# Kernel optimization log

Hardware: AMD Instinct MI355X
Metric: run time of the kernel (lower is better)

Reference implementation:

```python
import jax, jax.numpy as jnp
import numpy as np

B, T, C, H = 8, 2048, 384, 64

def setup_inputs() -> dict:
    key = jax.random.key(0)
    k1, k2, k3, k4 = jax.random.split(key, 4)
    x = jax.random.normal(k1, (B, T, C), dtype=jnp.float32)
    Wq = jax.random.normal(k2, (C, H), dtype=jnp.float32) * (C ** -0.5)
    Wk = jax.random.normal(k3, (C, H), dtype=jnp.float32) * (C ** -0.5)
    Wv = jax.random.normal(k4, (C, H), dtype=jnp.float32) * (C ** -0.5)
    return {"x": x, "Wq": Wq, "Wk": Wk, "Wv": Wv}

def reference(x, Wq, Wk, Wv):
    # x: (B, T, C); projections: (B, T, H)
    Bn, Tn, Cn = x.shape
    q = jnp.einsum('btc,ch->bth', x, Wq)
    k = jnp.einsum('btc,ch->bth', x, Wk)
    v = jnp.einsum('btc,ch->bth', x, Wv)
    # NOTE: source scales by C**-0.5 (embedding dim), not head_size**-0.5
    weights = jnp.einsum('bth,bsh->bts', q, k) * (Cn ** -0.5)  # (B, T, T)
    causal = jnp.tril(jnp.ones((Tn, Tn), dtype=bool))
    weights = jnp.where(causal, weights, -jnp.inf)
    # NOTE: source applies softmax over dim=1 (query/row axis), reproduced faithfully
    weights = jax.nn.softmax(weights, axis=1)
    # dropout omitted (eval-mode reference)
    return jnp.einsum('bts,bsh->bth', weights, v)
```

## Files before the change

kernel.cpp:

```cpp
#include <hip/hip_runtime.h>
#include <hip/hip_bf16.h>
#include <math.h>

#define Bn 8
#define Tn 2048
#define Cn 384
#define Hn 64
#define SCALE2 0.07362241f

using bf16x8 = __attribute__((ext_vector_type(8))) short;
using f32x4  = __attribute__((ext_vector_type(4))) float;
using u32x4  = __attribute__((ext_vector_type(4))) unsigned;

#define MFMA(a, b, c) __builtin_amdgcn_mfma_f32_16x16x32_bf16((a), (b), (c), 0, 0, 0)

static __device__ __forceinline__ short f2bf(float f) {
  unsigned u = __float_as_uint(f);
  u += 0x7fffu + ((u >> 16) & 1u);
  return (short)(u >> 16);
}
static __device__ __forceinline__ float bf2f(short s) {
  return __uint_as_float(((unsigned)(unsigned short)s) << 16);
}
static __device__ __forceinline__ float fexp2(float x) {
#if __has_builtin(__builtin_amdgcn_exp2f)
  return __builtin_amdgcn_exp2f(x);
#else
  return exp2f(x);
#endif
}
static __device__ __forceinline__ unsigned pack2(float lo, float hi) {
  return (unsigned)(unsigned short)f2bf(lo) | ((unsigned)(unsigned short)f2bf(hi) << 16);
}
static __device__ __forceinline__ bf16x8 ldp(const unsigned* p) {
  u32x4 t; t[0] = p[0]; t[1] = p[1]; t[2] = p[2]; t[3] = p[3];
  return __builtin_bit_cast(bf16x8, t);
}

__global__ __launch_bounds__(256) void wconv_kernel(
    const float* __restrict__ Wq, const float* __restrict__ Wk,
    const float* __restrict__ Wv, short* __restrict__ WbT) {
  int idx = blockIdx.x * 256 + threadIdx.x;
  int n = idx / 384, k = idx - n * 384;
  const float* W = (n < 64) ? Wq : (n < 128) ? Wk : Wv;
  WbT[idx] = f2bf(W[k * 64 + (n & 63)]);
}

__global__ __launch_bounds__(256) void proj_kernel(
    const float* __restrict__ x, const short* __restrict__ WbT,
    short* __restrict__ qb, short* __restrict__ kb, short* __restrict__ vT) {
  __shared__ short xs[16][392];
  __shared__ short vtile[64][20];
  const int tid = threadIdx.x;
  const int t0 = blockIdx.x * 16;
  const float* xb = x + (size_t)t0 * Cn;
  #pragma unroll
  for (int i = 0; i < 6; ++i) {
    int j = tid + i * 256;
    int row = j / 96, colv = (j - row * 96) * 4;
    float4 v = *(const float4*)(xb + row * Cn + colv);
    short4 s4; s4.x = f2bf(v.x); s4.y = f2bf(v.y); s4.z = f2bf(v.z); s4.w = f2bf(v.w);
    *(short4*)(&xs[row][colv]) = s4;
  }
  __syncthreads();
  const int w = tid >> 6, l15 = tid & 15, quad = (tid & 63) >> 4;
  f32x4 acc[3] = {};
  for (int ks = 0; ks < 12; ++ks) {
    bf16x8 a = *(const bf16x8*)(&xs[l15][ks * 32 + quad * 8]);
    #pragma unroll
    for (int cf = 0; cf < 3; ++cf) {
      bf16x8 bfr = *(const bf16x8*)(WbT + (size_t)(48 * w + 16 * cf + l15) * Cn + ks * 32 + quad * 8);
      acc[cf] = MFMA(a, bfr, acc[cf]);
    }
  }
  #pragma unroll
  for (int cf = 0; cf < 3; ++cf) {
    int cbase = 48 * w + 16 * cf, c = cbase + l15;
    #pragma unroll
    for (int r = 0; r < 4; ++r) {
      int row = t0 + quad * 4 + r;
      short val = f2bf(acc[cf][r]);
      if (cbase < 64)       qb[(size_t)row * Hn + c] = val;
      else if (cbase < 128) kb[(size_t)row * Hn + (c - 64)] = val;
      else                  vtile[c - 128][quad * 4 + r] = val;
    }
  }
  __syncthreads();
  const int b = t0 >> 11, t0l = t0 & 2047;
  int h = tid >> 2, tseg = (tid & 3) * 4;
  *(short4*)(vT + ((size_t)(b * Hn + h)) * Tn + t0l + tseg) =
      *(const short4*)(&vtile[h][tseg]);
}

__global__ __launch_bounds__(256) void colstats_kernel(
    const short* __restrict__ qb, const short* __restrict__ kb,
    float* __restrict__ pL) {
  const int unit = blockIdx.x;
  const int b = unit >> 7, rem = unit & 127;
  const int j = rem >> 3, u = rem & 7;
  const int lo = (u * 33) >> 3, hi = ((u + 1) * 33) >> 3;
  const int big = 32 - j;
  const int tid = threadIdx.x, w = tid >> 6, l15 = tid & 15, quad = (tid & 63) >> 4;
  __shared__ float redl[64][17];

  auto run = [&](const int i, const int k0, const int k1, const int slot) {
    const int s0 = i << 6;
    float l[4] = {0.f, 0.f, 0.f, 0.f};
    const int n = k1 - k0;
    if (n > 0) {
      bf16x8 bk[8];
      #pragma unroll
      for (int nf = 0; nf < 4; ++nf) {
        const size_t krow = (size_t)(b * Tn + s0 + 16 * nf + l15) * Hn;
        bk[2 * nf]     = *(const bf16x8*)(kb + krow + quad * 8);
        bk[2 * nf + 1] = *(const bf16x8*)(kb + krow + 32 + quad * 8);
      }
      auto cload = [&](bf16x8& A0, bf16x8& A1, int k) {
        size_t ar = (size_t)(b * Tn + ((i + k) << 6) + 16 * w + l15) * Hn;
        A0 = *(const bf16x8*)(qb + ar + quad * 8);
        A1 = *(const bf16x8*)(qb + ar + 32 + quad * 8);
      };
      auto ccomp = [&](bf16x8 A0, bf16x8 A1, int k) {
        f32x4 sc[4] = {};
        #pragma unroll
        for (int nf = 0; nf < 4; ++nf) {
          sc[nf] = MFMA(A0, bk[2 * nf], sc[nf]);
          sc[nf] = MFMA(A1, bk[2 * nf + 1], sc[nf]);
        }
        const bool diag = (k == 0);
        const int tb = ((i + k) << 6) + 16 * w + quad * 4;
        #pragma unroll
        for (int nf = 0; nf < 4; ++nf) {
          int s = s0 + 16 * nf + l15;
          #pragma unroll
          for (int r = 0; r < 4; ++r) {
            float v = sc[nf][r] * SCALE2;
            if (diag && (tb + r) < s) v = -INFINITY;
            l[nf] += fexp2(v);
          }
        }
      };
      bf16x8 a0A, a1A, a0B, a1B, a0C, a1C;
      cload(a0A, a1A, k0);
      if (n > 1) cload(a0B, a1B, k0 + 1);
      if (n > 2) cload(a0C, a1C, k0 + 2);
      int k = k0;
      while (k + 3 < k1) {
        ccomp(a0A, a1A, k);     cload(a0A, a1A, k + 3);
        ccomp(a0B, a1B, k + 1); if (k + 4 < k1) cload(a0B, a1B, k + 4);
        ccomp(a0C, a1C, k + 2); if (k + 5 < k1) cload(a0C, a1C, k + 5);
        k += 3;
      }
      const int rem2 = k1 - k;
      if (rem2 > 0) ccomp(a0A, a1A, k);
      if (rem2 > 1) ccomp(a0B, a1B, k + 1);
      if (rem2 > 2) ccomp(a0C, a1C, k + 2);
    }
    __syncthreads();
    #pragma unroll
    for (int nf = 0; nf < 4; ++nf) redl[16 * nf + l15][w * 4 + quad] = l[nf];
    __syncthreads();
    if (tid < 64) {
      float ls = 0.f;
      #pragma unroll
      for (int q2 = 0; q2 < 16; ++q2) ls += redl[tid][q2];
      pL[unit * 128 + slot * 64 + tid] = ls;
    }
  };
  run(j, lo, min(hi, big), 0);
  run(31 - j, max(lo, big) - big, hi - big, 1);
}

__global__ __launch_bounds__(256) void vhat_kernel(
    const short* __restrict__ vT, const float* __restrict__ pL,
    short* __restrict__ vS) {
  int gid = blockIdx.x * 256 + threadIdx.x;
  size_t base = (size_t)gid * 8;
  int b = (int)(base >> 17), s = (int)(base & 2047);
  int i = s >> 6, c = s & 63;
  int j2 = (i < 16) ? i : 31 - i;
  int slot = (i < 16) ? 0 : 1;
  const float* pp = pL + (size_t)((b * 16 + j2) * 8) * 128 + slot * 64 + c;
  float L0x = 0.f, L0y = 0.f, L0z = 0.f, L0w = 0.f;
  float L1x = 0.f, L1y = 0.f, L1z = 0.f, L1w = 0.f;
  #pragma unroll
  for (int u = 0; u < 8; ++u) {
    float4 p0 = *(const float4*)(pp + u * 128);
    float4 p1 = *(const float4*)(pp + u * 128 + 4);
    L0x += p0.x; L0y += p0.y; L0z += p0.z; L0w += p0.w;
    L1x += p1.x; L1y += p1.y; L1z += p1.z; L1w += p1.w;
  }
  short4 v0 = *(const short4*)(vT + base);
  short4 v1 = *(const short4*)(vT + base + 4);
  short4 r0, r1;
  r0.x = f2bf(bf2f(v0.x) / L0x); r0.y = f2bf(bf2f(v0.y) / L0y);
  r0.z = f2bf(bf2f(v0.z) / L0z); r0.w = f2bf(bf2f(v0.w) / L0w);
  r1.x = f2bf(bf2f(v1.x) / L1x); r1.y = f2bf(bf2f(v1.y) / L1y);
  r1.z = f2bf(bf2f(v1.z) / L1z); r1.w = f2bf(bf2f(v1.w) / L1w);
  *(short4*)(vS + base) = r0;
  *(short4*)(vS + base + 4) = r1;
}

__global__ __launch_bounds__(256, 2) void outg_kernel(
    const short* __restrict__ qb, const short* __restrict__ kb,
    const short* __restrict__ vS, float* __restrict__ out) {
  const int bid = blockIdx.x;
  const int tile = 31 - (bid >> 4);
  const int sub = bid & 15;
  const int b = sub >> 1, half = sub & 1;
  const int nch = tile + 1;
  const int tid = threadIdx.x, w = tid >> 6, l15 = tid & 15, quad = (tid & 63) >> 4;
  __shared__ unsigned plds[4][512];
  __shared__ float red[4][32][64];
  const int swz = (l15 & 7) << 4;
  int wroff[8];
  #pragma unroll
  for (int nf = 0; nf < 4; ++nf)
    #pragma unroll
    for (int p = 0; p < 2; ++p)
      wroff[2 * nf + p] = (l15 * 128 + ((nf * 32 + quad * 8 + p * 4) ^ swz)) >> 2;
  const int rd0 = (l15 * 128 + ((quad * 16) ^ swz)) >> 2;
  const int rd1 = (l15 * 128 + ((64 + quad * 16) ^ swz)) >> 2;
  const size_t QKbase = (size_t)b * Tn * Hn;
  const size_t Vbase  = (size_t)b * Hn * Tn;
  const int tbase = (tile << 6) + (half << 5);
  const int tg0 = tbase + l15;
  const int tg1 = tbase + 16 + l15;

  const size_t qrow0 = QKbase + (size_t)(tbase + l15) * Hn;
  const size_t qrow1 = qrow0 + 16 * Hn;
  const bf16x8 qf00 = *(const bf16x8*)(qb + qrow0 + quad * 8);
  const bf16x8 qf01 = *(const bf16x8*)(qb + qrow0 + 32 + quad * 8);
  const bf16x8 qf10 = *(const bf16x8*)(qb + qrow1 + quad * 8);
  const bf16x8 qf11 = *(const bf16x8*)(qb + qrow1 + 32 + quad * 8);

  f32x4 acc0[4] = {}, acc1[4] = {};
  bf16x8 kf[8], vf[8];
  auto loadK = [&](int ch) {
    const int s0 = ch << 6;
    #pragma unroll
    for (int nf = 0; nf < 4; ++nf) {
      const size_t kr = QKbase + (size_t)(s0 + 16 * nf + l15) * Hn;
      kf[2 * nf]     = *(const bf16x8*)(kb + kr + quad * 8);
      kf[2 * nf + 1] = *(const bf16x8*)(kb + kr + 32 + quad * 8);
    }
  };
  auto loadV = [&](int ch) {
    const int s0 = ch << 6;
    #pragma unroll
    for (int nf = 0; nf < 4; ++nf) {
      const size_t vr = Vbase + (size_t)(16 * nf + l15) * Tn + s0;
      vf[2 * nf]     = *(const bf16x8*)(vS + vr + quad * 8);
      vf[2 * nf + 1] = *(const bf16x8*)(vS + vr + 32 + quad * 8);
    }
  };
  auto strip = [&](const f32x4 (&sc)[4], int s0, bool diag, int tg, f32x4 (&acc)[4]) {
    #pragma unroll
    for (int nf = 0; nf < 4; ++nf) {
      float ev[4];
      #pragma unroll
      for (int r = 0; r < 4; ++r) {
        float v = sc[nf][r] * SCALE2;
        const int s = s0 + 16 * nf + quad * 4 + r;
        if (diag && tg < s) v = -INFINITY;
        ev[r] = fexp2(v);
      }
      plds[w][wroff[2 * nf]]     = pack2(ev[0], ev[1]);
      plds[w][wroff[2 * nf + 1]] = pack2(ev[2], ev[3]);
    }
    const bf16x8 a0 = ldp(&plds[w][rd0]);
    const bf16x8 a1 = ldp(&plds[w][rd1]);
    __builtin_amdgcn_s_setprio(1);
    #pragma unroll
    for (int nf = 0; nf < 4; ++nf) {
      acc[nf] = MFMA(a0, vf[2 * nf], acc[nf]);
      acc[nf] = MFMA(a1, vf[2 * nf + 1], acc[nf]);
    }
    __builtin_amdgcn_s_setprio(0);
  };

  if (w < nch) { loadK(w); loadV(w); }
  for (int ch = w; ch < nch; ch += 4) {
    const int s0 = ch << 6;
    f32x4 sc0[4] = {}, sc1[4] = {};
    __builtin_amdgcn_s_setprio(1);
    #pragma unroll
    for (int nf = 0; nf < 4; ++nf) {
      sc0[nf] = MFMA(kf[2 * nf], qf00, sc0[nf]);
      sc0[nf] = MFMA(kf[2 * nf + 1], qf01, sc0[nf]);
    }
    #pragma unroll
    for (int nf = 0; nf < 4; ++nf) {
      sc1[nf] = MFMA(kf[2 * nf], qf10, sc1[nf]);
      sc1[nf] = MFMA(kf[2 * nf + 1], qf11, sc1[nf]);
    }
    __builtin_amdgcn_s_setprio(0);
    const int nx = ch + 4;
    if (nx < nch) loadK(nx);
    const bool diag = (ch == tile);
    strip(sc0, s0, diag, tg0, acc0);
    strip(sc1, s0, diag, tg1, acc1);
    if (nx < nch) loadV(nx);
  }

  #pragma unroll
  for (int nf = 0; nf < 4; ++nf)
    #pragma unroll
    for (int r = 0; r < 4; ++r) {
      red[w][quad * 4 + r][16 * nf + l15]      = acc0[nf][r];
      red[w][16 + quad * 4 + r][16 * nf + l15] = acc1[nf][r];
    }
  __syncthreads();
  {
    const int row = tid >> 3, c8 = (tid & 7) * 8;
    float4 t0 = {0.f, 0.f, 0.f, 0.f}, t1 = {0.f, 0.f, 0.f, 0.f};
    #pragma unroll
    for (int ww = 0; ww < 4; ++ww) {
      float4 s0 = *(const float4*)(&red[ww][row][c8]);
      float4 s1 = *(const float4*)(&red[ww][row][c8 + 4]);
      t0.x += s0.x; t0.y += s0.y; t0.z += s0.z; t0.w += s0.w;
      t1.x += s1.x; t1.y += s1.y; t1.z += s1.z; t1.w += s1.w;
    }
    float* o = &out[QKbase + (size_t)(tbase + row) * Hn + c8];
    *(float4*)(o) = t0;
    *(float4*)(o + 4) = t1;
  }
}

extern "C" void kernel_launch(void* const* d_in, const int* in_sizes, int n_in,
                              void* d_out, int out_size, void* d_ws, size_t ws_size,
                              hipStream_t stream) {
  const float* x  = (const float*)d_in[0];
  const float* Wq = (const float*)d_in[1];
  const float* Wk = (const float*)d_in[2];
  const float* Wv = (const float*)d_in[3];
  char* ws = (char*)d_ws;
  short* qb   = (short*)(ws);
  short* kb   = (short*)(ws + 2097152);
  short* vT   = (short*)(ws + 4194304);
  short* vS   = (short*)(ws + 6291456);
  short* WbT  = (short*)(ws + 8388608);
  float* pL   = (float*)(ws + 8536064);
  float* outp = (float*)d_out;

  hipLaunchKernelGGL(wconv_kernel, dim3(288), dim3(256), 0, stream, Wq, Wk, Wv, WbT);
  hipLaunchKernelGGL(proj_kernel, dim3(Bn * Tn / 16), dim3(256), 0, stream, x, WbT, qb, kb, vT);
  hipLaunchKernelGGL(colstats_kernel, dim3(1024), dim3(256), 0, stream, qb, kb, pL);
  hipLaunchKernelGGL(vhat_kernel, dim3(512), dim3(256), 0, stream, vT, pL, vS);
  hipLaunchKernelGGL(outg_kernel, dim3(512), dim3(256), 0, stream, qb, kb, vS, outp);
}
```

Before: 137.5 us.

## Fuse column normalization into output kernel, drop vhat pass via atomic column sums

Drops the separate vhat kernel that rescaled V by the column sums. colstats now accumulates column sums directly into a zeroed Lsum buffer with atomics, and the output kernel loads the reciprocals into LDS and scales the exp values before packing. It also double-buffers the K fragments across chunk iterations and remaps the block order so batches are interleaved. This saves one launch and a full pass over V, at the cost of atomic contention, a 2048-float LDS array that may lower occupancy, and extra per-element multiplies.

```diff
diff --git a/kernel.cpp b/kernel.cpp
--- a/kernel.cpp
+++ b/kernel.cpp
@@ -29,6 +29,13 @@
   return exp2f(x);
 #endif
 }
+static __device__ __forceinline__ float frcp(float x) {
+#if __has_builtin(__builtin_amdgcn_rcpf)
+  return __builtin_amdgcn_rcpf(x);
+#else
+  return 1.0f / x;
+#endif
+}
 static __device__ __forceinline__ unsigned pack2(float lo, float hi) {
   return (unsigned)(unsigned short)f2bf(lo) | ((unsigned)(unsigned short)f2bf(hi) << 16);
 }
@@ -39,8 +46,10 @@
 
 __global__ __launch_bounds__(256) void wconv_kernel(
     const float* __restrict__ Wq, const float* __restrict__ Wk,
-    const float* __restrict__ Wv, short* __restrict__ WbT) {
+    const float* __restrict__ Wv, short* __restrict__ WbT,
+    float* __restrict__ Lsum) {
   int idx = blockIdx.x * 256 + threadIdx.x;
+  if (idx < Bn * Tn) Lsum[idx] = 0.f;
   int n = idx / 384, k = idx - n * 384;
   const float* W = (n < 64) ? Wq : (n < 128) ? Wk : Wv;
   WbT[idx] = f2bf(W[k * 64 + (n & 63)]);
@@ -94,8 +103,8 @@
 
 __global__ __launch_bounds__(256) void colstats_kernel(
     const short* __restrict__ qb, const short* __restrict__ kb,
-    float* __restrict__ pL) {
-  const int unit = blockIdx.x;
+    float* __restrict__ Lsum) {
+  const int unit = ((blockIdx.x & 7) << 7) | (blockIdx.x >> 3);
   const int b = unit >> 7, rem = unit & 127;
   const int j = rem >> 3, u = rem & 7;
   const int lo = (u * 33) >> 3, hi = ((u + 1) * 33) >> 3;
@@ -103,7 +112,7 @@
   const int tid = threadIdx.x, w = tid >> 6, l15 = tid & 15, quad = (tid & 63) >> 4;
   __shared__ float redl[64][17];
 
-  auto run = [&](const int i, const int k0, const int k1, const int slot) {
+  auto run = [&](const int i, const int k0, const int k1) {
     const int s0 = i << 6;
     float l[4] = {0.f, 0.f, 0.f, 0.f};
     const int n = k1 - k0;
@@ -164,54 +173,33 @@
       float ls = 0.f;
       #pragma unroll
       for (int q2 = 0; q2 < 16; ++q2) ls += redl[tid][q2];
-      pL[unit * 128 + slot * 64 + tid] = ls;
-    }
-  };
-  run(j, lo, min(hi, big), 0);
-  run(31 - j, max(lo, big) - big, hi - big, 1);
-}
-
-__global__ __launch_bounds__(256) void vhat_kernel(
-    const short* __restrict__ vT, const float* __restrict__ pL,
-    short* __restrict__ vS) {
-  int gid = blockIdx.x * 256 + threadIdx.x;
-  size_t base = (size_t)gid * 8;
-  int b = (int)(base >> 17), s = (int)(base & 2047);
-  int i = s >> 6, c = s & 63;
-  int j2 = (i < 16) ? i : 31 - i;
-  int slot = (i < 16) ? 0 : 1;
-  const float* pp = pL + (size_t)((b * 16 + j2) * 8) * 128 + slot * 64 + c;
-  float L0x = 0.f, L0y = 0.f, L0z = 0.f, L0w = 0.f;
-  float L1x = 0.f, L1y = 0.f, L1z = 0.f, L1w = 0.f;
-  #pragma unroll
-  for (int u = 0; u < 8; ++u) {
-    float4 p0 = *(const float4*)(pp + u * 128);
-    float4 p1 = *(const float4*)(pp + u * 128 + 4);
-    L0x += p0.x; L0y += p0.y; L0z += p0.z; L0w += p0.w;
-    L1x += p1.x; L1y += p1.y; L1z += p1.z; L1w += p1.w;
-  }
-  short4 v0 = *(const short4*)(vT + base);
-  short4 v1 = *(const short4*)(vT + base + 4);
-  short4 r0, r1;
-  r0.x = f2bf(bf2f(v0.x) / L0x); r0.y = f2bf(bf2f(v0.y) / L0y);
-  r0.z = f2bf(bf2f(v0.z) / L0z); r0.w = f2bf(bf2f(v0.w) / L0w);
-  r1.x = f2bf(bf2f(v1.x) / L1x); r1.y = f2bf(bf2f(v1.y) / L1y);
-  r1.z = f2bf(bf2f(v1.z) / L1z); r1.w = f2bf(bf2f(v1.w) / L1w);
-  *(short4*)(vS + base) = r0;
-  *(short4*)(vS + base + 4) = r1;
+      atomicAdd(&Lsum[b * Tn + s0 + tid], ls);
+    }
+  };
+  run(j, lo, min(hi, big));
+  run(31 - j, max(lo, big) - big, hi - big);
 }
 
 __global__ __launch_bounds__(256, 2) void outg_kernel(
     const short* __restrict__ qb, const short* __restrict__ kb,
-    const short* __restrict__ vS, float* __restrict__ out) {
+    const short* __restrict__ vT, const float* __restrict__ Lsum,
+    float* __restrict__ out) {
   const int bid = blockIdx.x;
-  const int tile = 31 - (bid >> 4);
-  const int sub = bid & 15;
-  const int b = sub >> 1, half = sub & 1;
+  const int b = bid & 7;
+  const int rest = bid >> 3;
+  const int tile = 31 - (rest >> 1);
+  const int half = rest & 1;
   const int nch = tile + 1;
   const int tid = threadIdx.x, w = tid >> 6, l15 = tid & 15, quad = (tid & 63) >> 4;
   __shared__ unsigned plds[4][512];
   __shared__ float red[4][32][64];
+  __shared__ float rcpl[2048];
+
+  const int smax = nch << 6;
+  for (int s = tid; s < smax; s += 256)
+    rcpl[s] = frcp(Lsum[b * Tn + s]);
+  __syncthreads();
+
   const int swz = (l15 & 7) << 4;
   int wroff[8];
   #pragma unroll
@@ -235,8 +223,8 @@
   const bf16x8 qf11 = *(const bf16x8*)(qb + qrow1 + 32 + quad * 8);
 
   f32x4 acc0[4] = {}, acc1[4] = {};
-  bf16x8 kf[8], vf[8];
-  auto loadK = [&](int ch) {
+  bf16x8 kfA[8], kfB[8], vf[8];
+  auto loadK = [&](bf16x8 (&kf)[8], int ch) {
     const int s0 = ch << 6;
     #pragma unroll
     for (int nf = 0; nf < 4; ++nf) {
@@ -250,11 +238,12 @@
     #pragma unroll
     for (int nf = 0; nf < 4; ++nf) {
       const size_t vr = Vbase + (size_t)(16 * nf + l15) * Tn + s0;
-      vf[2 * nf]     = *(const bf16x8*)(vS + vr + quad * 8);
-      vf[2 * nf + 1] = *(const bf16x8*)(vS + vr + 32 + quad * 8);
-    }
-  };
-  auto strip = [&](const f32x4 (&sc)[4], int s0, bool diag, int tg, f32x4 (&acc)[4]) {
+      vf[2 * nf]     = *(const bf16x8*)(vT + vr + quad * 8);
+      vf[2 * nf + 1] = *(const bf16x8*)(vT + vr + 32 + quad * 8);
+    }
+  };
+  auto strip = [&](const f32x4 (&sc)[4], const float (&rl)[16], int s0,
+                   bool diag, int tg, f32x4 (&acc)[4]) {
     #pragma unroll
     for (int nf = 0; nf < 4; ++nf) {
       float ev[4];
@@ -263,7 +252,7 @@
         float v = sc[nf][r] * SCALE2;
         const int s = s0 + 16 * nf + quad * 4 + r;
         if (diag && tg < s) v = -INFINITY;
-        ev[r] = fexp2(v);
+        ev[r] = fexp2(v) * rl[nf * 4 + r];
       }
       plds[w][wroff[2 * nf]]     = pack2(ev[0], ev[1]);
       plds[w][wroff[2 * nf + 1]] = pack2(ev[2], ev[3]);
@@ -278,29 +267,39 @@
     }
     __builtin_amdgcn_s_setprio(0);
   };
-
-  if (w < nch) { loadK(w); loadV(w); }
-  for (int ch = w; ch < nch; ch += 4) {
+  auto body = [&](int ch, const bf16x8 (&CUR)[8], bf16x8 (&NXT)[8]) {
     const int s0 = ch << 6;
+    const int nx = ch + 4;
     f32x4 sc0[4] = {}, sc1[4] = {};
     __builtin_amdgcn_s_setprio(1);
     #pragma unroll
     for (int nf = 0; nf < 4; ++nf) {
-      sc0[nf] = MFMA(kf[2 * nf], qf00, sc0[nf]);
-      sc0[nf] = MFMA(kf[2 * nf + 1], qf01, sc0[nf]);
-    }
-    #pragma unroll
-    for (int nf = 0; nf < 4; ++nf) {
-      sc1[nf] = MFMA(kf[2 * nf], qf10, sc1[nf]);
-      sc1[nf] = MFMA(kf[2 * nf + 1], qf11, sc1[nf]);
+      sc0[nf] = MFMA(CUR[2 * nf], qf00, sc0[nf]);
+      sc0[nf] = MFMA(CUR[2 * nf + 1], qf01, sc0[nf]);
+    }
+    #pragma unroll
+    for (int nf = 0; nf < 4; ++nf) {
+      sc1[nf] = MFMA(CUR[2 * nf], qf10, sc1[nf]);
+      sc1[nf] = MFMA(CUR[2 * nf + 1], qf11, sc1[nf]);
     }
     __builtin_amdgcn_s_setprio(0);
-    const int nx = ch + 4;
-    if (nx < nch) loadK(nx);
+    if (nx < nch) loadK(NXT, nx);
+    float rl[16];
+    #pragma unroll
+    for (int nf = 0; nf < 4; ++nf)
+      #pragma unroll
+      for (int r = 0; r < 4; ++r)
+        rl[nf * 4 + r] = rcpl[s0 + 16 * nf + quad * 4 + r];
     const bool diag = (ch == tile);
-    strip(sc0, s0, diag, tg0, acc0);
-    strip(sc1, s0, diag, tg1, acc1);
+    strip(sc0, rl, s0, diag, tg0, acc0);
+    strip(sc1, rl, s0, diag, tg1, acc1);
     if (nx < nch) loadV(nx);
+  };
+
+  if (w < nch) { loadK(kfA, w); loadV(w); }
+  for (int ch = w; ch < nch; ch += 8) {
+    body(ch, kfA, kfB);
+    if (ch + 4 < nch) body(ch + 4, kfB, kfA);
   }
 
   #pragma unroll
@@ -338,14 +337,12 @@
   short* qb   = (short*)(ws);
   short* kb   = (short*)(ws + 2097152);
   short* vT   = (short*)(ws + 4194304);
-  short* vS   = (short*)(ws + 6291456);
-  short* WbT  = (short*)(ws + 8388608);
-  float* pL   = (float*)(ws + 8536064);
+  short* WbT  = (short*)(ws + 6291456);
+  float* Lsum = (float*)(ws + 6438912);
   float* outp = (float*)d_out;
 
-  hipLaunchKernelGGL(wconv_kernel, dim3(288), dim3(256), 0, stream, Wq, Wk, Wv, WbT);
+  hipLaunchKernelGGL(wconv_kernel, dim3(288), dim3(256), 0, stream, Wq, Wk, Wv, WbT, Lsum);
   hipLaunchKernelGGL(proj_kernel, dim3(Bn * Tn / 16), dim3(256), 0, stream, x, WbT, qb, kb, vT);
-  hipLaunchKernelGGL(colstats_kernel, dim3(1024), dim3(256), 0, stream, qb, kb, pL);
-  hipLaunchKernelGGL(vhat_kernel, dim3(512), dim3(256), 0, stream, vT, pL, vS);
-  hipLaunchKernelGGL(outg_kernel, dim3(512), dim3(256), 0, stream, qb, kb, vS, outp);
-}
+  hipLaunchKernelGGL(colstats_kernel, dim3(1024), dim3(256), 0, stream, qb, kb, Lsum);
+  hipLaunchKernelGGL(outg_kernel, dim3(512), dim3(256), 0, stream, qb, kb, vT, Lsum, outp);
+}
```

Result: faster. 132.0 us (-4.0%).
